# Kernel tuning notes

Measured on AMD Instinct MI355X. Metric: run time of the kernel, lower is better.

The kernel has to match this reference:

```python
import jax, jax.numpy as jnp
import numpy as np

N_NODES = 100_000
N_EDGES = 3_200_000
F_IN = 64
HID = 16
N_CLASSES = 4


def setup_inputs() -> dict:
    key = jax.random.key(0)
    ks = jax.random.split(key, 9)
    x = jax.random.normal(ks[0], (N_NODES, F_IN), dtype=jnp.float32)
    edge_index = jax.random.randint(ks[1], (2, N_EDGES), 0, N_NODES, dtype=jnp.int64)
    edge_weight = jax.random.uniform(ks[2], (N_EDGES,), dtype=jnp.float32)
    # Glorot-style init for the three GCN layer weights, zero bias (PyG default)
    W1 = jax.random.normal(ks[3], (F_IN, HID), dtype=jnp.float32) * (1.0 / np.sqrt(F_IN))
    b1 = jnp.zeros((HID,), jnp.float32)
    W3 = jax.random.normal(ks[4], (HID, HID), dtype=jnp.float32) * (1.0 / np.sqrt(HID))
    b3 = jnp.zeros((HID,), jnp.float32)
    W2 = jax.random.normal(ks[5], (HID, N_CLASSES), dtype=jnp.float32) * (1.0 / np.sqrt(HID))
    b2 = jnp.zeros((N_CLASSES,), jnp.float32)
    return {"x": x, "edge_index": edge_index, "edge_weight": edge_weight,
            "W1": W1, "b1": b1, "W3": W3, "b3": b3, "W2": W2, "b2": b2}


def reference(x, edge_index, edge_weight, W1, b1, W3, b3, W2, b2):
    n = x.shape[0]
    # GCNConv default: add self-loops with weight 1, symmetric deg^-1/2 norm
    loop = jnp.arange(n, dtype=edge_index.dtype)
    row = jnp.concatenate([edge_index[0], loop])  # source nodes
    col = jnp.concatenate([edge_index[1], loop])  # target nodes
    ew = jnp.concatenate([edge_weight, jnp.ones((n,), edge_weight.dtype)])
    deg = jax.ops.segment_sum(ew, col, num_segments=n)
    dinv = jnp.where(deg > 0, jax.lax.rsqrt(deg), 0.0)
    norm = dinv[row] * ew * dinv[col]  # [E+N]

    def gcn_conv(h, W, b):
        h = h @ W                                  # [N, out] small matmul first
        msg = norm[:, None] * h[row]               # gather + scale, [E+N, out]
        return jax.ops.segment_sum(msg, col, num_segments=n) + b

    h = jax.nn.relu(gcn_conv(x, W1, b1))
    # dropout is identity in eval mode (training=False)
    h = jax.nn.relu(gcn_conv(h, W3, b3))
    h = gcn_conv(h, W2, b2)
    return jax.nn.log_softmax(h, axis=1)
```

## Files before the change

### kernel.cpp

```cpp
#include <hip/hip_runtime.h>
#include <math.h>

#define NN 100000
#define NE 3200000
#define F_IN 64
#define HID 16
#define NC 4

#define SZB 200
#define NB 500
#define CAP 7424
#define CH 8192
#define NCH 391
#define NW 16

typedef _Float16 half_t;
typedef _Float16 h4f __attribute__((ext_vector_type(4)));

__device__ __forceinline__ unsigned bdiv(unsigned c) {
    return (unsigned)(((unsigned long long)c * 167773ull) >> 25);
}

__device__ __forceinline__ float upw(int pk) {
    unsigned short us = (unsigned short)(pk & 0x7fff);
    half_t h;
    __builtin_memcpy(&h, &us, 2);
    return (float)h;
}

__global__ __launch_bounds__(1024) void k_bin(const int* __restrict__ row,
                                              const int* __restrict__ col,
                                              const float* __restrict__ ew,
                                              int* __restrict__ cursor,
                                              unsigned* __restrict__ bpk,
                                              unsigned char* __restrict__ bcl) {
    __shared__ int h[NB];
    __shared__ int lstart[NB];
    __shared__ int gbase[NB];
    __shared__ int wsum[16];
    __shared__ uint2 s2[CH];
    int tid = threadIdx.x;
    int lane = tid & 63, wv = tid >> 6;
    for (int i = tid; i < NB; i += 1024) h[i] = 0;
    __syncthreads();
    int e0 = blockIdx.x * CH;
    int e1 = min(e0 + CH, NE);
    int eCnt = e1 - e0;
    int4 c4s[2];
#pragma unroll
    for (int it = 0; it < 2; it++) {
        int i = e0 + tid * 4 + it * 4096;
        if (i < e1) {
            int4 c4 = *(const int4*)(col + i);
            c4s[it] = c4;
            atomicAdd(&h[bdiv(c4.x)], 1);
            atomicAdd(&h[bdiv(c4.y)], 1);
            atomicAdd(&h[bdiv(c4.z)], 1);
            atomicAdd(&h[bdiv(c4.w)], 1);
        }
    }
    __syncthreads();
    int c0 = (tid < NB) ? h[tid] : 0;
    int v = c0;
#pragma unroll
    for (int off = 1; off < 64; off <<= 1) {
        int t = __shfl_up(v, off, 64);
        if (lane >= off) v += t;
    }
    if (lane == 63) wsum[wv] = v;
    __syncthreads();
    if (tid < NB) {
        int pre = 0;
#pragma unroll
        for (int ww = 0; ww < 8; ww++) pre += (ww < wv) ? wsum[ww] : 0;
        int ex = (v + pre) - c0;
        lstart[tid] = ex;
        h[tid] = ex;
        if (c0) gbase[tid] = tid * CAP + atomicAdd(&cursor[tid], c0);
    }
    __syncthreads();
#pragma unroll
    for (int it = 0; it < 2; it++) {
        int i = e0 + tid * 4 + it * 4096;
        if (i < e1) {
            int4 c4 = c4s[it];
            int4 r4 = *(const int4*)(row + i);
            float4 w4 = *(const float4*)(ew + i);
            half_t hw0 = (half_t)w4.x, hw1 = (half_t)w4.y, hw2 = (half_t)w4.z, hw3 = (half_t)w4.w;
            unsigned short b0, b1, b2, b3;
            __builtin_memcpy(&b0, &hw0, 2); __builtin_memcpy(&b1, &hw1, 2);
            __builtin_memcpy(&b2, &hw2, 2); __builtin_memcpy(&b3, &hw3, 2);
            int p; unsigned bb;
            bb = bdiv(c4.x); p = atomicAdd(&h[bb], 1);
            s2[p] = make_uint2(((unsigned)r4.x << 15) | (b0 & 0x7fff),
                               (bb << 8) | (unsigned)(c4.x - 200u * bb));
            bb = bdiv(c4.y); p = atomicAdd(&h[bb], 1);
            s2[p] = make_uint2(((unsigned)r4.y << 15) | (b1 & 0x7fff),
                               (bb << 8) | (unsigned)(c4.y - 200u * bb));
            bb = bdiv(c4.z); p = atomicAdd(&h[bb], 1);
            s2[p] = make_uint2(((unsigned)r4.z << 15) | (b2 & 0x7fff),
                               (bb << 8) | (unsigned)(c4.z - 200u * bb));
            bb = bdiv(c4.w); p = atomicAdd(&h[bb], 1);
            s2[p] = make_uint2(((unsigned)r4.w << 15) | (b3 & 0x7fff),
                               (bb << 8) | (unsigned)(c4.w - 200u * bb));
        }
    }
    __syncthreads();
    for (int i = tid; i < eCnt; i += 1024) {
        uint2 e2 = s2[i];
        int lo = (int)(e2.y >> 8);
        int d = gbase[lo] + (i - lstart[lo]);
        if (d < (lo + 1) * CAP) {
            bpk[d] = e2.x;
            bcl[d] = (unsigned char)(e2.y & 255u);
        }
    }
}

__global__ __launch_bounds__(1024) void k_sort(const unsigned* __restrict__ bpk,
                                               const unsigned char* __restrict__ bcl,
                                               const int* __restrict__ cursor,
                                               const float* __restrict__ x,
                                               const float* __restrict__ W1,
                                               unsigned* __restrict__ epk,
                                               int2* __restrict__ nodeptr2,
                                               float* __restrict__ dinv,
                                               half_t* __restrict__ tt1) {
    __shared__ int hw[NW][SZB];
    __shared__ int cnt[SZB];
    __shared__ int ps[SZB];
    __shared__ int wsum4[4];
    __shared__ unsigned stage[CAP];
    __shared__ float Ws[F_IN * HID];
    int b = blockIdx.x, tid = threadIdx.x;
    int lane = tid & 63;
    int w = tid >> 6;
    for (int i = tid; i < NW * SZB; i += 1024) ((int*)hw)[i] = 0;
    for (int i = tid; i < F_IN * HID; i += 1024) Ws[i] = W1[i];
    __syncthreads();
    int s = b * CAP;
    int m = min(cursor[b], CAP);
    int e = s + m;
    for (int i = s + tid; i < e; i += 1024)
        atomicAdd(&hw[w][bcl[i]], 1);
    __syncthreads();
    if (tid < SZB) {
        int c = 0;
#pragma unroll
        for (int ww = 0; ww < NW; ww++) c += hw[ww][tid];
        cnt[tid] = c;
    }
    __syncthreads();
    int pc = (tid < SZB) ? ((cnt[tid] + 3) & ~3) : 0;
    int v = pc;
#pragma unroll
    for (int off = 1; off < 64; off <<= 1) {
        int t = __shfl_up(v, off, 64);
        if (lane >= off) v += t;
    }
    if (w < 4 && lane == 63) wsum4[w] = v;
    __syncthreads();
    if (tid < SZB) {
        int pre = 0;
#pragma unroll
        for (int ww = 0; ww < 4; ww++) pre += (ww < w) ? wsum4[ww] : 0;
        ps[tid] = v + pre;
    }
    __syncthreads();
    if (tid < SZB) {
        int run = ps[tid] - pc;
#pragma unroll
        for (int ww = 0; ww < NW; ww++) {
            int t = hw[ww][tid];
            hw[ww][tid] = run;
            run += t;
        }
    }
    __syncthreads();
    int mpad = min(ps[SZB - 1], CAP);
    for (int i = tid; i < mpad; i += 1024) stage[i] = 0u;
    __syncthreads();
    for (int i = s + tid; i < e; i += 1024) {
        int cl = bcl[i];
        int pos = atomicAdd(&hw[w][cl], 1);
        if (pos < CAP) stage[pos] = bpk[i];
    }
    __syncthreads();
    for (int i = tid; i < mpad; i += 1024) epk[s + i] = stage[i];
    int nl = tid >> 2, l = tid & 3;
    float di = 0.0f;
    int n = b * SZB + nl;
    if (nl < SZB) {
        int pcn = (cnt[nl] + 3) & ~3;
        int ex = ps[nl] - pcn;
        float sw = 0.0f;
        for (int i = ex + l; i < ex + pcn; i += 4) sw += upw((int)stage[i]);
        sw += __shfl_xor(sw, 1, 4);
        sw += __shfl_xor(sw, 2, 4);
        di = rsqrtf(1.0f + sw);
        if (n < NN && l == 0) {
            nodeptr2[n] = make_int2(s + ex, s + ex + pcn);
            dinv[n] = di;
        }
    }
    if (nl < SZB && n < NN) {
        float part[HID];
#pragma unroll
        for (int j = 0; j < HID; j++) part[j] = 0.0f;
        const float4* xp = (const float4*)(x + (size_t)n * F_IN) + l * 4;
#pragma unroll
        for (int k4 = 0; k4 < 4; k4++) {
            float4 vx = xp[k4];
            int k = l * 16 + k4 * 4;
#pragma unroll
            for (int j = 0; j < HID; j++) {
                part[j] += vx.x * Ws[(k + 0) * HID + j];
                part[j] += vx.y * Ws[(k + 1) * HID + j];
                part[j] += vx.z * Ws[(k + 2) * HID + j];
                part[j] += vx.w * Ws[(k + 3) * HID + j];
            }
        }
#pragma unroll
        for (int j = 0; j < HID; j++) {
            part[j] += __shfl_xor(part[j], 1, 4);
            part[j] += __shfl_xor(part[j], 2, 4);
        }
        h4f o;
        o.x = (half_t)(di * part[4 * l + 0]);
        o.y = (half_t)(di * part[4 * l + 1]);
        o.z = (half_t)(di * part[4 * l + 2]);
        o.w = (half_t)(di * part[4 * l + 3]);
        ((h4f*)tt1)[n * 4 + l] = o;
    }
}

#define ACC4(Q, V0, V1, V2, V3)                                                 \
    do {                                                                        \
        float w0 = upw((Q).x), w1 = upw((Q).y), w2 = upw((Q).z), w3 = upw((Q).w); \
        ax += w0 * (float)(V0).x; ay += w0 * (float)(V0).y;                     \
        az += w0 * (float)(V0).z; aw += w0 * (float)(V0).w;                     \
        ax += w1 * (float)(V1).x; ay += w1 * (float)(V1).y;                     \
        az += w1 * (float)(V1).z; aw += w1 * (float)(V1).w;                     \
        ax += w2 * (float)(V2).x; ay += w2 * (float)(V2).y;                     \
        az += w2 * (float)(V2).z; aw += w2 * (float)(V2).w;                     \
        ax += w3 * (float)(V3).x; ay += w3 * (float)(V3).y;                     \
        az += w3 * (float)(V3).z; aw += w3 * (float)(V3).w;                     \
    } while (0)

__device__ __forceinline__ void half_range(int px, int py, int h, int& b0, int& b1) {
    int chunks = (py - px) >> 2;
    int c0 = (chunks + 1) >> 1;
    b0 = px + ((h == 0) ? 0 : c0 * 4);
    b1 = (h == 0) ? (px + c0 * 4) : py;
}

template <int DN>
__global__ __launch_bounds__(256) void k_aggf(const unsigned* __restrict__ epk,
                                              const int2* __restrict__ nptr,
                                              const half_t* __restrict__ tt_in,
                                              const float* __restrict__ bias,
                                              const float* __restrict__ dinv,
                                              const float* __restrict__ Wn,
                                              half_t* __restrict__ tt_out) {
    __shared__ float Ws[HID * DN];
    if (threadIdx.x < HID * DN) Ws[threadIdx.x] = Wn[threadIdx.x];
    __syncthreads();
    int tid = blockIdx.x * 256 + threadIdx.x;
    int n = tid >> 3;
    int l = (tid >> 1) & 3;
    l = tid & 3;
    int h = (tid >> 2) & 1;
    if (n >= NN) return;
    int2 p = nptr[n];
    const h4f* ttp = (const h4f*)tt_in;
    h4f sv = ttp[n * 4 + l];
    float ax = 0.f, ay = 0.f, az = 0.f, aw = 0.f;
    int base, pend;
    half_range(p.x, p.y, h, base, pend);
    if (base < pend) {
        int4 q = *(const int4*)(epk + base);
        base += 4;
        bool more = base < pend;
        int4 qn = *(const int4*)(epk + (more ? base : p.x));
        h4f v0 = ttp[((((unsigned)q.x) >> 15) << 2) + l];
        h4f v1 = ttp[((((unsigned)q.y) >> 15) << 2) + l];
        h4f v2 = ttp[((((unsigned)q.z) >> 15) << 2) + l];
        h4f v3 = ttp[((((unsigned)q.w) >> 15) << 2) + l];
        while (more) {
            base += 4;
            bool more2 = base < pend;
            int4 qnn = *(const int4*)(epk + (more2 ? base : p.x));
            h4f u0 = ttp[((((unsigned)qn.x) >> 15) << 2) + l];
            h4f u1 = ttp[((((unsigned)qn.y) >> 15) << 2) + l];
            h4f u2 = ttp[((((unsigned)qn.z) >> 15) << 2) + l];
            h4f u3 = ttp[((((unsigned)qn.w) >> 15) << 2) + l];
            ACC4(q, v0, v1, v2, v3);
            q = qn; qn = qnn;
            v0 = u0; v1 = u1; v2 = u2; v3 = u3;
            more = more2;
        }
        ACC4(q, v0, v1, v2, v3);
    }
    ax += __shfl_xor(ax, 4, 8);
    ay += __shfl_xor(ay, 4, 8);
    az += __shfl_xor(az, 4, 8);
    aw += __shfl_xor(aw, 4, 8);
    float di = dinv[n];
    const float4* b4p = (const float4*)bias;
    float4 b4 = b4p[l];
    float hreg[4];
    hreg[0] = fmaxf(b4.x + di * (ax + (float)sv.x), 0.f);
    hreg[1] = fmaxf(b4.y + di * (ay + (float)sv.y), 0.f);
    hreg[2] = fmaxf(b4.z + di * (az + (float)sv.z), 0.f);
    hreg[3] = fmaxf(b4.w + di * (aw + (float)sv.w), 0.f);
    if (DN == 16) {
        float ox = 0.f, oy = 0.f, oz = 0.f, ow = 0.f;
#pragma unroll
        for (int k = 0; k < HID; k++) {
            float hk = __shfl(hreg[k & 3], k >> 2, 4);
            const float4 wk = *(const float4*)&Ws[k * 16 + 4 * l];
            ox += hk * wk.x; oy += hk * wk.y; oz += hk * wk.z; ow += hk * wk.w;
        }
        if (h == 0) {
            h4f ov;
            ov.x = (half_t)(di * ox); ov.y = (half_t)(di * oy);
            ov.z = (half_t)(di * oz); ov.w = (half_t)(di * ow);
            ((h4f*)tt_out)[n * 4 + l] = ov;
        }
    } else {
        float o = 0.f;
#pragma unroll
        for (int k = 0; k < HID; k++) {
            float hk = __shfl(hreg[k & 3], k >> 2, 4);
            o += hk * Ws[k * DN + l];
        }
        if (h == 0) tt_out[(size_t)n * DN + l] = (half_t)(di * o);
    }
}

__global__ __launch_bounds__(256) void k_agg4sm(const unsigned* __restrict__ epk,
                                                const int2* __restrict__ nptr,
                                                const half_t* __restrict__ tt,
                                                const float* __restrict__ bias,
                                                const float* __restrict__ dinv,
                                                float* __restrict__ out) {
    int tid = blockIdx.x * 256 + threadIdx.x;
    int n = tid >> 3;
    int l = tid & 3;
    int h = (tid >> 2) & 1;
    if (n >= NN) return;
    int2 p = nptr[n];
    float self = (float)tt[n * 4 + l];
    float acc = 0.f;
    int base, pend;
    half_range(p.x, p.y, h, base, pend);
    if (base < pend) {
        int4 q = *(const int4*)(epk + base);
        base += 4;
        bool more = base < pend;
        int4 qn = *(const int4*)(epk + (more ? base : p.x));
        float v0 = (float)tt[((((unsigned)q.x) >> 15) << 2) + l];
        float v1 = (float)tt[((((unsigned)q.y) >> 15) << 2) + l];
        float v2 = (float)tt[((((unsigned)q.z) >> 15) << 2) + l];
        float v3 = (float)tt[((((unsigned)q.w) >> 15) << 2) + l];
        while (more) {
            base += 4;
            bool more2 = base < pend;
            int4 qnn = *(const int4*)(epk + (more2 ? base : p.x));
            float u0 = (float)tt[((((unsigned)qn.x) >> 15) << 2) + l];
            float u1 = (float)tt[((((unsigned)qn.y) >> 15) << 2) + l];
            float u2 = (float)tt[((((unsigned)qn.z) >> 15) << 2) + l];
            float u3 = (float)tt[((((unsigned)qn.w) >> 15) << 2) + l];
            acc += upw(q.x) * v0;
            acc += upw(q.y) * v1;
            acc += upw(q.z) * v2;
            acc += upw(q.w) * v3;
            q = qn; qn = qnn;
            v0 = u0; v1 = u1; v2 = u2; v3 = u3;
            more = more2;
        }
        acc += upw(q.x) * v0;
        acc += upw(q.y) * v1;
        acc += upw(q.z) * v2;
        acc += upw(q.w) * v3;
    }
    acc += __shfl_xor(acc, 4, 8);
    float di = dinv[n];
    float logit = bias[l] + di * (acc + self);
    float mx = logit;
    mx = fmaxf(mx, __shfl_xor(mx, 1, 4));
    mx = fmaxf(mx, __shfl_xor(mx, 2, 4));
    float ex = expf(logit - mx);
    float sm = ex;
    sm += __shfl_xor(sm, 1, 4);
    sm += __shfl_xor(sm, 2, 4);
    if (h == 0) out[n * 4 + l] = logit - mx - logf(sm);
}

extern "C" void kernel_launch(void* const* d_in, const int* in_sizes, int n_in,
                              void* d_out, int out_size, void* d_ws, size_t ws_size,
                              hipStream_t stream) {
    const float* x  = (const float*)d_in[0];
    const int*   ei = (const int*)d_in[1];
    const float* ew = (const float*)d_in[2];
    const float* W1 = (const float*)d_in[3];
    const float* b1 = (const float*)d_in[4];
    const float* W3 = (const float*)d_in[5];
    const float* b3 = (const float*)d_in[6];
    const float* W2 = (const float*)d_in[7];
    const float* b2 = (const float*)d_in[8];
    float* out = (float*)d_out;

    const int* row = ei;
    const int* col = ei + NE;

    const size_t NEP = (size_t)NB * CAP;
    char* ws = (char*)d_ws;
    size_t off = 0;
    float*         dinv     = (float*)(ws + off);         off += 400000;
    int2*          nodeptr2 = (int2*)(ws + off);          off += 800000;
    int*           cursor   = (int*)(ws + off);           off += 2048;
    unsigned*      epk      = (unsigned*)(ws + off);      off += NEP * 4;
    unsigned*      bpk      = (unsigned*)(ws + off);      off += NEP * 4;
    unsigned char* bcl      = (unsigned char*)(ws + off); off += (NEP + 15) & ~15ull;
    half_t*        tt1      = (half_t*)(ws + off);        off += (size_t)NN * HID * 2;
    half_t*        tt2      = (half_t*)(ws + off);        off += (size_t)NN * HID * 2;
    half_t*        tt3      = (half_t*)(ws + off);        off += (size_t)NN * NC * 2;

    hipMemsetAsync(cursor, 0, NB * sizeof(int), stream);

    k_bin<<<NCH, 1024, 0, stream>>>(row, col, ew, cursor, bpk, bcl);
    k_sort<<<NB, 1024, 0, stream>>>(bpk, bcl, cursor, x, W1, epk, nodeptr2, dinv, tt1);

    int gA8 = (NN * 8 + 255) / 256;

    k_aggf<HID><<<gA8, 256, 0, stream>>>(epk, nodeptr2, tt1, b1, dinv, W3, tt2);
    k_aggf<NC><<<gA8, 256, 0, stream>>>(epk, nodeptr2, tt2, b3, dinv, W2, tt3);
    k_agg4sm<<<gA8, 256, 0, stream>>>(epk, nodeptr2, tt3, b2, dinv, out);
}
```

Baseline: 210.5 us.

## Split edges across eight lanes per node, each gathering full feature rows

Restructures the aggregation kernels so each of the 8 lanes assigned to a node walks a strided subset of edge chunks and gathers the whole 16-wide (or 4-wide) fp16 feature row per edge. Previously the lanes split features 4-wide across a 2-way edge split. This gives more edge-level parallelism per node and full-row 32-byte gathers, at the cost of more accumulator registers and a 3-stage shuffle reduction. The software prefetch pipeline is dropped, and the final log-softmax is computed by one lane and written as a float4.

```diff
diff --git a/kernel.cpp b/kernel.cpp
--- a/kernel.cpp
+++ b/kernel.cpp
@@ -15,7 +15,9 @@
 #define NW 16
 
 typedef _Float16 half_t;
+typedef _Float16 h2f __attribute__((ext_vector_type(2)));
 typedef _Float16 h4f __attribute__((ext_vector_type(4)));
+typedef _Float16 h8f __attribute__((ext_vector_type(8)));
 
 __device__ __forceinline__ unsigned bdiv(unsigned c) {
     return (unsigned)(((unsigned long long)c * 167773ull) >> 25);
@@ -234,26 +236,6 @@
     }
 }
 
-#define ACC4(Q, V0, V1, V2, V3)                                                 \
-    do {                                                                        \
-        float w0 = upw((Q).x), w1 = upw((Q).y), w2 = upw((Q).z), w3 = upw((Q).w); \
-        ax += w0 * (float)(V0).x; ay += w0 * (float)(V0).y;                     \
-        az += w0 * (float)(V0).z; aw += w0 * (float)(V0).w;                     \
-        ax += w1 * (float)(V1).x; ay += w1 * (float)(V1).y;                     \
-        az += w1 * (float)(V1).z; aw += w1 * (float)(V1).w;                     \
-        ax += w2 * (float)(V2).x; ay += w2 * (float)(V2).y;                     \
-        az += w2 * (float)(V2).z; aw += w2 * (float)(V2).w;                     \
-        ax += w3 * (float)(V3).x; ay += w3 * (float)(V3).y;                     \
-        az += w3 * (float)(V3).z; aw += w3 * (float)(V3).w;                     \
-    } while (0)
-
-__device__ __forceinline__ void half_range(int px, int py, int h, int& b0, int& b1) {
-    int chunks = (py - px) >> 2;
-    int c0 = (chunks + 1) >> 1;
-    b0 = px + ((h == 0) ? 0 : c0 * 4);
-    b1 = (h == 0) ? (px + c0 * 4) : py;
-}
-
 template <int DN>
 __global__ __launch_bounds__(256) void k_aggf(const unsigned* __restrict__ epk,
                                               const int2* __restrict__ nptr,
@@ -263,78 +245,78 @@
                                               const float* __restrict__ Wn,
                                               half_t* __restrict__ tt_out) {
     __shared__ float Ws[HID * DN];
+    __shared__ float bs[DN];
     if (threadIdx.x < HID * DN) Ws[threadIdx.x] = Wn[threadIdx.x];
+    if (threadIdx.x < DN) bs[threadIdx.x] = bias[threadIdx.x];
     __syncthreads();
     int tid = blockIdx.x * 256 + threadIdx.x;
     int n = tid >> 3;
-    int l = (tid >> 1) & 3;
-    l = tid & 3;
-    int h = (tid >> 2) & 1;
+    int h = tid & 7;
     if (n >= NN) return;
     int2 p = nptr[n];
-    const h4f* ttp = (const h4f*)tt_in;
-    h4f sv = ttp[n * 4 + l];
-    float ax = 0.f, ay = 0.f, az = 0.f, aw = 0.f;
-    int base, pend;
-    half_range(p.x, p.y, h, base, pend);
-    if (base < pend) {
+    const h8f* t8 = (const h8f*)tt_in;
+    float acc[HID];
+#pragma unroll
+    for (int j = 0; j < HID; j++) acc[j] = 0.0f;
+    for (int base = p.x + h * 4; base < p.y; base += 32) {
         int4 q = *(const int4*)(epk + base);
-        base += 4;
-        bool more = base < pend;
-        int4 qn = *(const int4*)(epk + (more ? base : p.x));
-        h4f v0 = ttp[((((unsigned)q.x) >> 15) << 2) + l];
-        h4f v1 = ttp[((((unsigned)q.y) >> 15) << 2) + l];
-        h4f v2 = ttp[((((unsigned)q.z) >> 15) << 2) + l];
-        h4f v3 = ttp[((((unsigned)q.w) >> 15) << 2) + l];
-        while (more) {
-            base += 4;
-            bool more2 = base < pend;
-            int4 qnn = *(const int4*)(epk + (more2 ? base : p.x));
-            h4f u0 = ttp[((((unsigned)qn.x) >> 15) << 2) + l];
-            h4f u1 = ttp[((((unsigned)qn.y) >> 15) << 2) + l];
-            h4f u2 = ttp[((((unsigned)qn.z) >> 15) << 2) + l];
-            h4f u3 = ttp[((((unsigned)qn.w) >> 15) << 2) + l];
-            ACC4(q, v0, v1, v2, v3);
-            q = qn; qn = qnn;
-            v0 = u0; v1 = u1; v2 = u2; v3 = u3;
-            more = more2;
-        }
-        ACC4(q, v0, v1, v2, v3);
-    }
-    ax += __shfl_xor(ax, 4, 8);
-    ay += __shfl_xor(ay, 4, 8);
-    az += __shfl_xor(az, 4, 8);
-    aw += __shfl_xor(aw, 4, 8);
+        {
+            float wq = upw(q.x); int r = ((unsigned)q.x) >> 15;
+            h8f a = t8[r * 2], b = t8[r * 2 + 1];
+#pragma unroll
+            for (int j = 0; j < 8; j++) { acc[j] += wq * (float)a[j]; acc[8 + j] += wq * (float)b[j]; }
+        }
+        {
+            float wq = upw(q.y); int r = ((unsigned)q.y) >> 15;
+            h8f a = t8[r * 2], b = t8[r * 2 + 1];
+#pragma unroll
+            for (int j = 0; j < 8; j++) { acc[j] += wq * (float)a[j]; acc[8 + j] += wq * (float)b[j]; }
+        }
+        {
+            float wq = upw(q.z); int r = ((unsigned)q.z) >> 15;
+            h8f a = t8[r * 2], b = t8[r * 2 + 1];
+#pragma unroll
+            for (int j = 0; j < 8; j++) { acc[j] += wq * (float)a[j]; acc[8 + j] += wq * (float)b[j]; }
+        }
+        {
+            float wq = upw(q.w); int r = ((unsigned)q.w) >> 15;
+            h8f a = t8[r * 2], b = t8[r * 2 + 1];
+#pragma unroll
+            for (int j = 0; j < 8; j++) { acc[j] += wq * (float)a[j]; acc[8 + j] += wq * (float)b[j]; }
+        }
+    }
+#pragma unroll
+    for (int j = 0; j < HID; j++) {
+        acc[j] += __shfl_xor(acc[j], 1, 8);
+        acc[j] += __shfl_xor(acc[j], 2, 8);
+        acc[j] += __shfl_xor(acc[j], 4, 8);
+    }
     float di = dinv[n];
-    const float4* b4p = (const float4*)bias;
-    float4 b4 = b4p[l];
-    float hreg[4];
-    hreg[0] = fmaxf(b4.x + di * (ax + (float)sv.x), 0.f);
-    hreg[1] = fmaxf(b4.y + di * (ay + (float)sv.y), 0.f);
-    hreg[2] = fmaxf(b4.z + di * (az + (float)sv.z), 0.f);
-    hreg[3] = fmaxf(b4.w + di * (aw + (float)sv.w), 0.f);
+    h8f s0 = t8[n * 2], s1 = t8[n * 2 + 1];
+    float hv[HID];
+#pragma unroll
+    for (int j = 0; j < 8; j++) {
+        hv[j]     = fmaxf(bs[(DN == 16) ? j : 0] * 0.0f + bias[j] + di * (acc[j] + (float)s0[j]), 0.f);
+        hv[8 + j] = fmaxf(bias[8 + j] + di * (acc[8 + j] + (float)s1[j]), 0.f);
+    }
     if (DN == 16) {
-        float ox = 0.f, oy = 0.f, oz = 0.f, ow = 0.f;
+        float o0 = 0.f, o1 = 0.f;
 #pragma unroll
         for (int k = 0; k < HID; k++) {
-            float hk = __shfl(hreg[k & 3], k >> 2, 4);
-            const float4 wk = *(const float4*)&Ws[k * 16 + 4 * l];
-            ox += hk * wk.x; oy += hk * wk.y; oz += hk * wk.z; ow += hk * wk.w;
-        }
-        if (h == 0) {
-            h4f ov;
-            ov.x = (half_t)(di * ox); ov.y = (half_t)(di * oy);
-            ov.z = (half_t)(di * oz); ov.w = (half_t)(di * ow);
-            ((h4f*)tt_out)[n * 4 + l] = ov;
-        }
+            o0 += hv[k] * Ws[k * 16 + 2 * h];
+            o1 += hv[k] * Ws[k * 16 + 2 * h + 1];
+        }
+        h2f ov;
+        ov.x = (half_t)(di * o0);
+        ov.y = (half_t)(di * o1);
+        ((h2f*)tt_out)[n * 8 + h] = ov;
     } else {
-        float o = 0.f;
-#pragma unroll
-        for (int k = 0; k < HID; k++) {
-            float hk = __shfl(hreg[k & 3], k >> 2, 4);
-            o += hk * Ws[k * DN + l];
-        }
-        if (h == 0) tt_out[(size_t)n * DN + l] = (half_t)(di * o);
+        if (h < DN) {
+            float o = 0.f;
+#pragma unroll
+            for (int k = 0; k < HID; k++) o += hv[k] * Ws[k * DN + h];
+            tt_out[(size_t)n * DN + h] = (half_t)(di * o);
+        }
     }
 }
 
@@ -346,55 +328,50 @@
                                                 float* __restrict__ out) {
     int tid = blockIdx.x * 256 + threadIdx.x;
     int n = tid >> 3;
-    int l = tid & 3;
-    int h = (tid >> 2) & 1;
+    int h = tid & 7;
     if (n >= NN) return;
     int2 p = nptr[n];
-    float self = (float)tt[n * 4 + l];
-    float acc = 0.f;
-    int base, pend;
-    half_range(p.x, p.y, h, base, pend);
-    if (base < pend) {
+    const h4f* t4 = (const h4f*)tt;
+    float a0 = 0.f, a1 = 0.f, a2 = 0.f, a3 = 0.f;
+    for (int base = p.x + h * 4; base < p.y; base += 32) {
         int4 q = *(const int4*)(epk + base);
-        base += 4;
-        bool more = base < pend;
-        int4 qn = *(const int4*)(epk + (more ? base : p.x));
-        float v0 = (float)tt[((((unsigned)q.x) >> 15) << 2) + l];
-        float v1 = (float)tt[((((unsigned)q.y) >> 15) << 2) + l];
-        float v2 = (float)tt[((((unsigned)q.z) >> 15) << 2) + l];
-        float v3 = (float)tt[((((unsigned)q.w) >> 15) << 2) + l];
-        while (more) {
-            base += 4;
-            bool more2 = base < pend;
-            int4 qnn = *(const int4*)(epk + (more2 ? base : p.x));
-            float u0 = (float)tt[((((unsigned)qn.x) >> 15) << 2) + l];
-            float u1 = (float)tt[((((unsigned)qn.y) >> 15) << 2) + l];
-            float u2 = (float)tt[((((unsigned)qn.z) >> 15) << 2) + l];
-            float u3 = (float)tt[((((unsigned)qn.w) >> 15) << 2) + l];
-            acc += upw(q.x) * v0;
-            acc += upw(q.y) * v1;
-            acc += upw(q.z) * v2;
-            acc += upw(q.w) * v3;
-            q = qn; qn = qnn;
-            v0 = u0; v1 = u1; v2 = u2; v3 = u3;
-            more = more2;
-        }
-        acc += upw(q.x) * v0;
-        acc += upw(q.y) * v1;
-        acc += upw(q.z) * v2;
-        acc += upw(q.w) * v3;
-    }
-    acc += __shfl_xor(acc, 4, 8);
-    float di = dinv[n];
-    float logit = bias[l] + di * (acc + self);
-    float mx = logit;
-    mx = fmaxf(mx, __shfl_xor(mx, 1, 4));
-    mx = fmaxf(mx, __shfl_xor(mx, 2, 4));
-    float ex = expf(logit - mx);
-    float sm = ex;
-    sm += __shfl_xor(sm, 1, 4);
-    sm += __shfl_xor(sm, 2, 4);
-    if (h == 0) out[n * 4 + l] = logit - mx - logf(sm);
+        {
+            float wq = upw(q.x); h4f v = t4[((unsigned)q.x) >> 15];
+            a0 += wq * (float)v.x; a1 += wq * (float)v.y; a2 += wq * (float)v.z; a3 += wq * (float)v.w;
+        }
+        {
+            float wq = upw(q.y); h4f v = t4[((unsigned)q.y) >> 15];
+            a0 += wq * (float)v.x; a1 += wq * (float)v.y; a2 += wq * (float)v.z; a3 += wq * (float)v.w;
+        }
+        {
+            float wq = upw(q.z); h4f v = t4[((unsigned)q.z) >> 15];
+            a0 += wq * (float)v.x; a1 += wq * (float)v.y; a2 += wq * (float)v.z; a3 += wq * (float)v.w;
+        }
+        {
+            float wq = upw(q.w); h4f v = t4[((unsigned)q.w) >> 15];
+            a0 += wq * (float)v.x; a1 += wq * (float)v.y; a2 += wq * (float)v.z; a3 += wq * (float)v.w;
+        }
+    }
+#pragma unroll
+    for (int off = 1; off < 8; off <<= 1) {
+        a0 += __shfl_xor(a0, off, 8);
+        a1 += __shfl_xor(a1, off, 8);
+        a2 += __shfl_xor(a2, off, 8);
+        a3 += __shfl_xor(a3, off, 8);
+    }
+    if (h == 0) {
+        float di = dinv[n];
+        h4f sv = t4[n];
+        float l0 = bias[0] + di * (a0 + (float)sv.x);
+        float l1 = bias[1] + di * (a1 + (float)sv.y);
+        float l2 = bias[2] + di * (a2 + (float)sv.z);
+        float l3 = bias[3] + di * (a3 + (float)sv.w);
+        float mx = fmaxf(fmaxf(l0, l1), fmaxf(l2, l3));
+        float sm = expf(l0 - mx) + expf(l1 - mx) + expf(l2 - mx) + expf(l3 - mx);
+        float lse = mx + logf(sm);
+        float4 o = make_float4(l0 - lse, l1 - lse, l2 - lse, l3 - lse);
+        ((float4*)out)[n] = o;
+    }
 }
 
 extern "C" void kernel_launch(void* const* d_in, const int* in_sizes, int n_in,
```

After: 227.1 us. 7.9% more time.

## Interleave edge halves and deepen gather prefetch pipeline in aggregation kernels

Applied to the files above, without the earlier changes.

The aggregation kernels now split each node's edge list between the two half-threads in interleaved groups of four instead of as two contiguous halves. The software pipeline also goes from one to two groups of gathers in flight, which adds latency hiding for the random feature loads. The binning chunk size and chunk count change as well. The deeper pipeline needs more registers, which may lower occupancy, and it adds a redundant final prefetch load.

```diff
diff --git a/kernel.cpp b/kernel.cpp
--- a/kernel.cpp
+++ b/kernel.cpp
@@ -10,8 +10,8 @@
 #define SZB 200
 #define NB 500
 #define CAP 7424
-#define CH 8192
-#define NCH 391
+#define CH 6400
+#define NCH 500
 #define NW 16
 
 typedef _Float16 half_t;
@@ -247,13 +247,6 @@
         az += w3 * (float)(V3).z; aw += w3 * (float)(V3).w;                     \
     } while (0)
 
-__device__ __forceinline__ void half_range(int px, int py, int h, int& b0, int& b1) {
-    int chunks = (py - px) >> 2;
-    int c0 = (chunks + 1) >> 1;
-    b0 = px + ((h == 0) ? 0 : c0 * 4);
-    b1 = (h == 0) ? (px + c0 * 4) : py;
-}
-
 template <int DN>
 __global__ __launch_bounds__(256) void k_aggf(const unsigned* __restrict__ epk,
                                               const int2* __restrict__ nptr,
@@ -267,39 +260,46 @@
     __syncthreads();
     int tid = blockIdx.x * 256 + threadIdx.x;
     int n = tid >> 3;
-    int l = (tid >> 1) & 3;
-    l = tid & 3;
+    int l = tid & 3;
     int h = (tid >> 2) & 1;
     if (n >= NN) return;
     int2 p = nptr[n];
     const h4f* ttp = (const h4f*)tt_in;
     h4f sv = ttp[n * 4 + l];
     float ax = 0.f, ay = 0.f, az = 0.f, aw = 0.f;
-    int base, pend;
-    half_range(p.x, p.y, h, base, pend);
-    if (base < pend) {
-        int4 q = *(const int4*)(epk + base);
-        base += 4;
-        bool more = base < pend;
-        int4 qn = *(const int4*)(epk + (more ? base : p.x));
-        h4f v0 = ttp[((((unsigned)q.x) >> 15) << 2) + l];
-        h4f v1 = ttp[((((unsigned)q.y) >> 15) << 2) + l];
-        h4f v2 = ttp[((((unsigned)q.z) >> 15) << 2) + l];
-        h4f v3 = ttp[((((unsigned)q.w) >> 15) << 2) + l];
-        while (more) {
-            base += 4;
-            bool more2 = base < pend;
-            int4 qnn = *(const int4*)(epk + (more2 ? base : p.x));
-            h4f u0 = ttp[((((unsigned)qn.x) >> 15) << 2) + l];
-            h4f u1 = ttp[((((unsigned)qn.y) >> 15) << 2) + l];
-            h4f u2 = ttp[((((unsigned)qn.z) >> 15) << 2) + l];
-            h4f u3 = ttp[((((unsigned)qn.w) >> 15) << 2) + l];
-            ACC4(q, v0, v1, v2, v3);
-            q = qn; qn = qnn;
+    int b = p.x + h * 4;
+    const int pend = p.y;
+    if (b < pend) {
+        int4 q0 = *(const int4*)(epk + b);
+        int nb = b + 8;
+        bool f1 = nb < pend;
+        int4 q1 = *(const int4*)(epk + (f1 ? nb : p.x));
+        h4f v0 = ttp[((((unsigned)q0.x) >> 15) << 2) + l];
+        h4f v1 = ttp[((((unsigned)q0.y) >> 15) << 2) + l];
+        h4f v2 = ttp[((((unsigned)q0.z) >> 15) << 2) + l];
+        h4f v3 = ttp[((((unsigned)q0.w) >> 15) << 2) + l];
+        nb += 8;
+        bool f2 = f1 && (nb < pend);
+        int4 q2 = *(const int4*)(epk + (f2 ? nb : p.x));
+        h4f u0 = ttp[((((unsigned)q1.x) >> 15) << 2) + l];
+        h4f u1 = ttp[((((unsigned)q1.y) >> 15) << 2) + l];
+        h4f u2 = ttp[((((unsigned)q1.z) >> 15) << 2) + l];
+        h4f u3 = ttp[((((unsigned)q1.w) >> 15) << 2) + l];
+        while (f1) {
+            h4f w0 = ttp[((((unsigned)q2.x) >> 15) << 2) + l];
+            h4f w1 = ttp[((((unsigned)q2.y) >> 15) << 2) + l];
+            h4f w2 = ttp[((((unsigned)q2.z) >> 15) << 2) + l];
+            h4f w3 = ttp[((((unsigned)q2.w) >> 15) << 2) + l];
+            nb += 8;
+            bool f3 = f2 && (nb < pend);
+            int4 qn = *(const int4*)(epk + (f3 ? nb : p.x));
+            ACC4(q0, v0, v1, v2, v3);
+            q0 = q1; q1 = q2; q2 = qn;
             v0 = u0; v1 = u1; v2 = u2; v3 = u3;
-            more = more2;
-        }
-        ACC4(q, v0, v1, v2, v3);
+            u0 = w0; u1 = w1; u2 = w2; u3 = w3;
+            f1 = f2; f2 = f3;
+        }
+        ACC4(q0, v0, v1, v2, v3);
     }
     ax += __shfl_xor(ax, 4, 8);
     ay += __shfl_xor(ay, 4, 8);
@@ -352,37 +352,45 @@
     int2 p = nptr[n];
     float self = (float)tt[n * 4 + l];
     float acc = 0.f;
-    int base, pend;
-    half_range(p.x, p.y, h, base, pend);
-    if (base < pend) {
-        int4 q = *(const int4*)(epk + base);
-        base += 4;
-        bool more = base < pend;
-        int4 qn = *(const int4*)(epk + (more ? base : p.x));
-        float v0 = (float)tt[((((unsigned)q.x) >> 15) << 2) + l];
-        float v1 = (float)tt[((((unsigned)q.y) >> 15) << 2) + l];
-        float v2 = (float)tt[((((unsigned)q.z) >> 15) << 2) + l];
-        float v3 = (float)tt[((((unsigned)q.w) >> 15) << 2) + l];
-        while (more) {
-            base += 4;
-            bool more2 = base < pend;
-            int4 qnn = *(const int4*)(epk + (more2 ? base : p.x));
-            float u0 = (float)tt[((((unsigned)qn.x) >> 15) << 2) + l];
-            float u1 = (float)tt[((((unsigned)qn.y) >> 15) << 2) + l];
-            float u2 = (float)tt[((((unsigned)qn.z) >> 15) << 2) + l];
-            float u3 = (float)tt[((((unsigned)qn.w) >> 15) << 2) + l];
-            acc += upw(q.x) * v0;
-            acc += upw(q.y) * v1;
-            acc += upw(q.z) * v2;
-            acc += upw(q.w) * v3;
-            q = qn; qn = qnn;
+    int b = p.x + h * 4;
+    const int pend = p.y;
+    if (b < pend) {
+        int4 q0 = *(const int4*)(epk + b);
+        int nb = b + 8;
+        bool f1 = nb < pend;
+        int4 q1 = *(const int4*)(epk + (f1 ? nb : p.x));
+        float v0 = (float)tt[((((unsigned)q0.x) >> 15) << 2) + l];
+        float v1 = (float)tt[((((unsigned)q0.y) >> 15) << 2) + l];
+        float v2 = (float)tt[((((unsigned)q0.z) >> 15) << 2) + l];
+        float v3 = (float)tt[((((unsigned)q0.w) >> 15) << 2) + l];
+        nb += 8;
+        bool f2 = f1 && (nb < pend);
+        int4 q2 = *(const int4*)(epk + (f2 ? nb : p.x));
+        float u0 = (float)tt[((((unsigned)q1.x) >> 15) << 2) + l];
+        float u1 = (float)tt[((((unsigned)q1.y) >> 15) << 2) + l];
+        float u2 = (float)tt[((((unsigned)q1.z) >> 15) << 2) + l];
+        float u3 = (float)tt[((((unsigned)q1.w) >> 15) << 2) + l];
+        while (f1) {
+            float w0 = (float)tt[((((unsigned)q2.x) >> 15) << 2) + l];
+            float w1 = (float)tt[((((unsigned)q2.y) >> 15) << 2) + l];
+            float w2 = (float)tt[((((unsigned)q2.z) >> 15) << 2) + l];
+            float w3 = (float)tt[((((unsigned)q2.w) >> 15) << 2) + l];
+            nb += 8;
+            bool f3 = f2 && (nb < pend);
+            int4 qn = *(const int4*)(epk + (f3 ? nb : p.x));
+            acc += upw(q0.x) * v0;
+            acc += upw(q0.y) * v1;
+            acc += upw(q0.z) * v2;
+            acc += upw(q0.w) * v3;
+            q0 = q1; q1 = q2; q2 = qn;
             v0 = u0; v1 = u1; v2 = u2; v3 = u3;
-            more = more2;
-        }
-        acc += upw(q.x) * v0;
-        acc += upw(q.y) * v1;
-        acc += upw(q.z) * v2;
-        acc += upw(q.w) * v3;
+            u0 = w0; u1 = w1; u2 = w2; u3 = w3;
+            f1 = f2; f2 = f3;
+        }
+        acc += upw(q0.x) * v0;
+        acc += upw(q0.y) * v1;
+        acc += upw(q0.z) * v2;
+        acc += upw(q0.w) * v3;
     }
     acc += __shfl_xor(acc, 4, 8);
     float di = dinv[n];
```

Result: no change. 210.8 us (+0.1%).

## Split each node's edge list across four interleaved lanes groups and rebalance binning chunks

Applied to the files above, without the earlier changes.

The aggregation kernels now assign 16 threads per node instead of 8, with four groups striding through the edge list in interleaved 4-edge chunks rather than two contiguous halves, followed by a two-step shuffle reduction. This gives more memory-level parallelism per node for the gather-heavy SpMM passes. The binning kernel chunk size changes so that the launch grid matches the number of buckets. The cost is twice as many threads, more idle lanes on low-degree nodes, and extra shuffle work.

```diff
diff --git a/kernel.cpp b/kernel.cpp
--- a/kernel.cpp
+++ b/kernel.cpp
@@ -10,8 +10,8 @@
 #define SZB 200
 #define NB 500
 #define CAP 7424
-#define CH 8192
-#define NCH 391
+#define CH 6400
+#define NCH 500
 #define NW 16
 
 typedef _Float16 half_t;
@@ -247,13 +247,6 @@
         az += w3 * (float)(V3).z; aw += w3 * (float)(V3).w;                     \
     } while (0)
 
-__device__ __forceinline__ void half_range(int px, int py, int h, int& b0, int& b1) {
-    int chunks = (py - px) >> 2;
-    int c0 = (chunks + 1) >> 1;
-    b0 = px + ((h == 0) ? 0 : c0 * 4);
-    b1 = (h == 0) ? (px + c0 * 4) : py;
-}
-
 template <int DN>
 __global__ __launch_bounds__(256) void k_aggf(const unsigned* __restrict__ epk,
                                               const int2* __restrict__ nptr,
@@ -266,20 +259,19 @@
     if (threadIdx.x < HID * DN) Ws[threadIdx.x] = Wn[threadIdx.x];
     __syncthreads();
     int tid = blockIdx.x * 256 + threadIdx.x;
-    int n = tid >> 3;
-    int l = (tid >> 1) & 3;
-    l = tid & 3;
-    int h = (tid >> 2) & 1;
+    int n = tid >> 4;
+    int l = tid & 3;
+    int h = (tid >> 2) & 3;
     if (n >= NN) return;
     int2 p = nptr[n];
     const h4f* ttp = (const h4f*)tt_in;
     h4f sv = ttp[n * 4 + l];
     float ax = 0.f, ay = 0.f, az = 0.f, aw = 0.f;
-    int base, pend;
-    half_range(p.x, p.y, h, base, pend);
+    int base = p.x + h * 4;
+    const int pend = p.y;
     if (base < pend) {
         int4 q = *(const int4*)(epk + base);
-        base += 4;
+        base += 16;
         bool more = base < pend;
         int4 qn = *(const int4*)(epk + (more ? base : p.x));
         h4f v0 = ttp[((((unsigned)q.x) >> 15) << 2) + l];
@@ -287,7 +279,7 @@
         h4f v2 = ttp[((((unsigned)q.z) >> 15) << 2) + l];
         h4f v3 = ttp[((((unsigned)q.w) >> 15) << 2) + l];
         while (more) {
-            base += 4;
+            base += 16;
             bool more2 = base < pend;
             int4 qnn = *(const int4*)(epk + (more2 ? base : p.x));
             h4f u0 = ttp[((((unsigned)qn.x) >> 15) << 2) + l];
@@ -301,10 +293,14 @@
         }
         ACC4(q, v0, v1, v2, v3);
     }
-    ax += __shfl_xor(ax, 4, 8);
-    ay += __shfl_xor(ay, 4, 8);
-    az += __shfl_xor(az, 4, 8);
-    aw += __shfl_xor(aw, 4, 8);
+    ax += __shfl_xor(ax, 4, 16);
+    ay += __shfl_xor(ay, 4, 16);
+    az += __shfl_xor(az, 4, 16);
+    aw += __shfl_xor(aw, 4, 16);
+    ax += __shfl_xor(ax, 8, 16);
+    ay += __shfl_xor(ay, 8, 16);
+    az += __shfl_xor(az, 8, 16);
+    aw += __shfl_xor(aw, 8, 16);
     float di = dinv[n];
     const float4* b4p = (const float4*)bias;
     float4 b4 = b4p[l];
@@ -345,18 +341,18 @@
                                                 const float* __restrict__ dinv,
                                                 float* __restrict__ out) {
     int tid = blockIdx.x * 256 + threadIdx.x;
-    int n = tid >> 3;
+    int n = tid >> 4;
     int l = tid & 3;
-    int h = (tid >> 2) & 1;
+    int h = (tid >> 2) & 3;
     if (n >= NN) return;
     int2 p = nptr[n];
     float self = (float)tt[n * 4 + l];
     float acc = 0.f;
-    int base, pend;
-    half_range(p.x, p.y, h, base, pend);
+    int base = p.x + h * 4;
+    const int pend = p.y;
     if (base < pend) {
         int4 q = *(const int4*)(epk + base);
-        base += 4;
+        base += 16;
         bool more = base < pend;
         int4 qn = *(const int4*)(epk + (more ? base : p.x));
         float v0 = (float)tt[((((unsigned)q.x) >> 15) << 2) + l];
@@ -364,7 +360,7 @@
         float v2 = (float)tt[((((unsigned)q.z) >> 15) << 2) + l];
         float v3 = (float)tt[((((unsigned)q.w) >> 15) << 2) + l];
         while (more) {
-            base += 4;
+            base += 16;
             bool more2 = base < pend;
             int4 qnn = *(const int4*)(epk + (more2 ? base : p.x));
             float u0 = (float)tt[((((unsigned)qn.x) >> 15) << 2) + l];
@@ -384,7 +380,8 @@
         acc += upw(q.z) * v2;
         acc += upw(q.w) * v3;
     }
-    acc += __shfl_xor(acc, 4, 8);
+    acc += __shfl_xor(acc, 4, 16);
+    acc += __shfl_xor(acc, 8, 16);
     float di = dinv[n];
     float logit = bias[l] + di * (acc + self);
     float mx = logit;
@@ -432,9 +429,9 @@
     k_bin<<<NCH, 1024, 0, stream>>>(row, col, ew, cursor, bpk, bcl);
     k_sort<<<NB, 1024, 0, stream>>>(bpk, bcl, cursor, x, W1, epk, nodeptr2, dinv, tt1);
 
-    int gA8 = (NN * 8 + 255) / 256;
-
-    k_aggf<HID><<<gA8, 256, 0, stream>>>(epk, nodeptr2, tt1, b1, dinv, W3, tt2);
-    k_aggf<NC><<<gA8, 256, 0, stream>>>(epk, nodeptr2, tt2, b3, dinv, W2, tt3);
-    k_agg4sm<<<gA8, 256, 0, stream>>>(epk, nodeptr2, tt3, b2, dinv, out);
-}
+    int gA16 = (NN * 16 + 255) / 256;
+
+    k_aggf<HID><<<gA16, 256, 0, stream>>>(epk, nodeptr2, tt1, b1, dinv, W3, tt2);
+    k_aggf<NC><<<gA16, 256, 0, stream>>>(epk, nodeptr2, tt2, b3, dinv, W2, tt3);
+    k_agg4sm<<<gA16, 256, 0, stream>>>(epk, nodeptr2, tt3, b2, dinv, out);
+}
```

Result: no change. 208.4 us (-1.0%).
